# Kernel optimization log

Hardware: AMD Instinct MI355X
Metric: run time of the kernel (lower is better)

Reference implementation:

```python
import jax, jax.numpy as jnp
import numpy as np

NEG = -1e30  # log-zero surrogate (avoid -inf for stable grads)


def ctc_neg_log_like(log_probs, targets, input_lengths, target_lengths):
    """Standard CTC (blank=0) negative log-likelihood, mean over batch.
    Math-equivalent to k2 topo-compile + intersect_dense + log-semiring tot_scores.
    log_probs: [B,T,C] logits or log-probs (re-normalized, as GradExpNormalize does).
    """
    lp = jax.nn.log_softmax(log_probs, axis=-1)
    B, T, C = lp.shape
    S = targets.shape[1]
    L = 2 * S + 1  # blank-interleaved extended label sequence length
    ext = jnp.zeros((B, L), jnp.int32).at[:, 1::2].set(targets.astype(jnp.int32))
    prev2 = jnp.pad(ext[:, :-2], ((0, 0), (2, 0)), constant_values=-1)
    can_skip = (ext != prev2) & (ext != 0)  # skip transition allowed

    lp_tb = jnp.moveaxis(lp, 1, 0)  # [T,B,C] for scan over time
    start = jnp.full((B, L), NEG, lp.dtype).at[:, 0].set(0.0).at[:, 1].set(0.0)
    alpha0 = start + jnp.take_along_axis(lp_tb[0], ext, axis=1)  # [B,L]

    def step(alpha, xs):
        lp_t, t = xs
        emit_t = jnp.take_along_axis(lp_t, ext, axis=1)  # [B,L]
        s1 = jnp.pad(alpha[:, :-1], ((0, 0), (1, 0)), constant_values=NEG)
        s2 = jnp.where(can_skip,
                       jnp.pad(alpha[:, :-2], ((0, 0), (2, 0)), constant_values=NEG),
                       NEG)
        new = jnp.logaddexp(jnp.logaddexp(alpha, s1), s2) + emit_t
        # freeze alpha once past this utterance's length
        new = jnp.where((t < input_lengths)[:, None], new, alpha)
        return new, None

    ts = jnp.arange(1, T, dtype=jnp.int32)
    alpha, _ = jax.lax.scan(step, alpha0, (lp_tb[1:], ts))

    idx1 = (2 * target_lengths).astype(jnp.int32)
    idx2 = jnp.maximum(2 * target_lengths - 1, 0).astype(jnp.int32)
    a1 = jnp.take_along_axis(alpha, idx1[:, None], axis=1)[:, 0]
    a2 = jnp.take_along_axis(alpha, idx2[:, None], axis=1)[:, 0]
    a2 = jnp.where(target_lengths > 0, a2, NEG)
    tot_scores = jnp.logaddexp(a1, a2)  # per-utterance log-likelihood
    return -jnp.mean(tot_scores)  # reduction='mean'


def setup_inputs() -> dict:
    key = jax.random.key(0)
    k1, k2, k3, k4 = jax.random.split(key, 4)
    B, T, C, S = 64, 2048, 1024, 256
    log_probs = jax.random.normal(k1, (B, T, C), dtype=jnp.float32)
    targets = 1 + jax.random.randint(k2, (B, S), 0, C - 1, dtype=jnp.int32)  # labels in [1, C)
    input_lengths = jax.random.randint(k3, (B,), T // 2, T + 1, dtype=jnp.int32)
    target_lengths = jax.random.randint(k4, (B,), S // 2, S + 1, dtype=jnp.int32)
    return {"log_probs": log_probs, "targets": targets,
            "input_lengths": input_lengths, "target_lengths": target_lengths}


def reference(log_probs, targets, input_lengths, target_lengths):
    return ctc_neg_log_like(log_probs, targets, input_lengths, target_lengths)
```

## Files before the change

kernel.cpp:

```cpp
#include <hip/hip_runtime.h>
#include <math.h>

typedef __attribute__((ext_vector_type(4))) float f32x4;

#define SB() __builtin_amdgcn_sched_barrier(0)
#define WAITV(n)                                              \
  do {                                                        \
    asm volatile("s_waitcnt vmcnt(" #n ")" ::: "memory");     \
    SB();                                                     \
  } while (0)
#define LD4(dst, ptr, OFF)                                           \
  asm volatile("global_load_dwordx4 %0, %1, off offset:" OFF         \
               : "=v"(dst) : "v"(ptr) : "memory")
#define LD1(dst, ptr, OFF)                                           \
  asm volatile("global_load_dword %0, %1, off offset:" OFF           \
               : "=v"(dst) : "v"(ptr) : "memory")

__device__ inline float wave_max64(float v) {
#pragma unroll
  for (int off = 32; off > 0; off >>= 1) v = fmaxf(v, __shfl_xor(v, off, 64));
  return v;
}
__device__ inline float wave_sum64(float v) {
#pragma unroll
  for (int off = 32; off > 0; off >>= 1) v += __shfl_xor(v, off, 64);
  return v;
}
__device__ inline float wave_max_dpp(float x) {
  int xi = __float_as_int(x);
  x = fmaxf(x, __int_as_float(__builtin_amdgcn_update_dpp(xi, xi, 0x111, 0xf, 0xf, false)));
  xi = __float_as_int(x);
  x = fmaxf(x, __int_as_float(__builtin_amdgcn_update_dpp(xi, xi, 0x112, 0xf, 0xf, false)));
  xi = __float_as_int(x);
  x = fmaxf(x, __int_as_float(__builtin_amdgcn_update_dpp(xi, xi, 0x114, 0xf, 0xf, false)));
  xi = __float_as_int(x);
  x = fmaxf(x, __int_as_float(__builtin_amdgcn_update_dpp(xi, xi, 0x118, 0xf, 0xf, false)));
  xi = __float_as_int(x);
  x = fmaxf(x, __int_as_float(__builtin_amdgcn_update_dpp(xi, xi, 0x142, 0xa, 0xf, false)));
  xi = __float_as_int(x);
  x = fmaxf(x, __int_as_float(__builtin_amdgcn_update_dpp(xi, xi, 0x143, 0xc, 0xf, false)));
  return __int_as_float(__builtin_amdgcn_readlane(__float_as_int(x), 63));
}
__device__ inline float lane_shr1(float x) {
  return __int_as_float(__builtin_amdgcn_update_dpp(
      0, __float_as_int(x), 0x138, 0xf, 0xf, true));
}

__global__ __launch_bounds__(256) void k1_gather(
    const float* __restrict__ lp, const int* __restrict__ targets,
    float* __restrict__ gw, int t0, int T, int Tc, int RB, int S) {
  __shared__ __align__(16) float rowbuf4[4][1024];
  const int w = threadIdx.x >> 6;
  const int lane = threadIdx.x & 63;
  const int tloc = blockIdx.x * 4 + w;
  const int b = blockIdx.y;
  const int t = t0 + tloc;
  const int4 tg4 = *(const int4*)(targets + (size_t)b * S + 4 * lane);
  float* rowbuf = rowbuf4[w];

  const float* row = lp + ((size_t)b * T + t) * 1024;
  const float4 v0 = *(const float4*)(row + 4 * lane);
  const float4 v1 = *(const float4*)(row + 256 + 4 * lane);
  const float4 v2 = *(const float4*)(row + 512 + 4 * lane);
  const float4 v3 = *(const float4*)(row + 768 + 4 * lane);
  float mx = fmaxf(fmaxf(fmaxf(v0.x, v0.y), fmaxf(v0.z, v0.w)),
                   fmaxf(fmaxf(v1.x, v1.y), fmaxf(v1.z, v1.w)));
  mx = fmaxf(mx, fmaxf(fmaxf(fmaxf(v2.x, v2.y), fmaxf(v2.z, v2.w)),
                       fmaxf(fmaxf(v3.x, v3.y), fmaxf(v3.z, v3.w))));
  mx = wave_max64(mx);
  float sm = __expf(v0.x - mx) + __expf(v0.y - mx) + __expf(v0.z - mx) +
             __expf(v0.w - mx) + __expf(v1.x - mx) + __expf(v1.y - mx) +
             __expf(v1.z - mx) + __expf(v1.w - mx) + __expf(v2.x - mx) +
             __expf(v2.y - mx) + __expf(v2.z - mx) + __expf(v2.w - mx) +
             __expf(v3.x - mx) + __expf(v3.y - mx) + __expf(v3.z - mx) +
             __expf(v3.w - mx);
  sm = wave_sum64(sm);
  const float lse = mx + __logf(sm);
  *(float4*)(rowbuf + 4 * lane) = v0;
  *(float4*)(rowbuf + 256 + 4 * lane) = v1;
  *(float4*)(rowbuf + 512 + 4 * lane) = v2;
  *(float4*)(rowbuf + 768 + 4 * lane) = v3;
  const float e0 = __expf(rowbuf[tg4.x] - lse);
  const float e1 = __expf(rowbuf[tg4.y] - lse);
  const float e2 = __expf(rowbuf[tg4.z] - lse);
  const float e3 = __expf(rowbuf[tg4.w] - lse);
  float* gr = gw + ((size_t)b * RB + tloc) * 264;
  *(float4*)(gr + 4 * lane) = make_float4(e0, e1, e2, e3);
  if (lane == 0) gr[256] = __expf(rowbuf[0] - lse);
}

#define DECL8(P)                                                     \
  f32x4 P##v0, P##v1, P##v2, P##v3, P##v4, P##v5, P##v6, P##v7;      \
  float P##q0, P##q1, P##q2, P##q3, P##q4, P##q5, P##q6, P##q7;

#define ISS8(P)                                                      \
  do {                                                               \
    LD4(P##v0, gpA_, "0");    LD1(P##q0, gqA_, "0");                 \
    LD4(P##v1, gpA_, "1056"); LD1(P##q1, gqA_, "1056");              \
    LD4(P##v2, gpA_, "2112"); LD1(P##q2, gqA_, "2112");              \
    LD4(P##v3, gpA_, "3168"); LD1(P##q3, gqA_, "3168");              \
    LD4(P##v4, gpB_, "0");    LD1(P##q4, gqB_, "0");                 \
    LD4(P##v5, gpB_, "1056"); LD1(P##q5, gqB_, "1056");              \
    LD4(P##v6, gpB_, "2112"); LD1(P##q6, gqB_, "2112");              \
    LD4(P##v7, gpB_, "3168"); LD1(P##q7, gqB_, "3168");              \
    gpA_ += 2112; gqA_ += 2112; gpB_ += 2112; gqB_ += 2112;          \
  } while (0)

#define KSR(pv, qv)                                              \
  {                                                              \
    const float hm1 = lane_shr1(a7);                             \
    const float n0 = (a0 + hm1) * (qv);                          \
    const float n1 = __fmaf_rn(sk1, hm1, a1 + a0) * (pv).x;      \
    const float n2 = (a2 + a1) * (qv);                           \
    const float n3 = __fmaf_rn(sk3, a1, a3 + a2) * (pv).y;       \
    const float n4 = (a4 + a3) * (qv);                           \
    const float n5 = __fmaf_rn(sk5, a3, a5 + a4) * (pv).z;       \
    const float n6 = (a6 + a5) * (qv);                           \
    const float n7 = __fmaf_rn(sk7, a5, a7 + a6) * (pv).w;       \
    const float n8 = (a8 + a7) * (qv);                           \
    a0 = n0; a1 = n1; a2 = n2; a3 = n3; a4 = n4;                 \
    a5 = n5; a6 = n6; a7 = n7; a8 = n8;                          \
  }

#define RESC()                                                            \
  {                                                                       \
    float m_ = fmaxf(fmaxf(fmaxf(fmaxf(a0, a1), fmaxf(a2, a3)),           \
                           fmaxf(fmaxf(a4, a5), fmaxf(a6, a7))), a8);     \
    m_ = wave_max_dpp(m_);                                                \
    const int e_ =                                                        \
        (m_ > 0.f) ? (int)((__float_as_uint(m_) >> 23) & 255u) - 127 : 0; \
    a0 = ldexpf(a0, -e_); a1 = ldexpf(a1, -e_); a2 = ldexpf(a2, -e_);     \
    a3 = ldexpf(a3, -e_); a4 = ldexpf(a4, -e_); a5 = ldexpf(a5, -e_);     \
    a6 = ldexpf(a6, -e_); a7 = ldexpf(a7, -e_); a8 = ldexpf(a8, -e_);     \
    E += e_;                                                              \
  }

#define COMP8(P, rem)                                            \
  do {                                                           \
    if ((rem) >= 8) {                                            \
      KSR(P##v0, P##q0) KSR(P##v1, P##q1) KSR(P##v2, P##q2)      \
      KSR(P##v3, P##q3) KSR(P##v4, P##q4) KSR(P##v5, P##q5)      \
      KSR(P##v6, P##q6) KSR(P##v7, P##q7) RESC()                 \
    } else {                                                     \
      KSR(P##v0, P##q0)                                          \
      if ((rem) > 1) KSR(P##v1, P##q1)                           \
      if ((rem) > 2) KSR(P##v2, P##q2)                           \
      if ((rem) > 3) KSR(P##v3, P##q3)                           \
      if ((rem) > 4) KSR(P##v4, P##q4)                           \
      if ((rem) > 5) KSR(P##v5, P##q5)                           \
      if ((rem) > 6) KSR(P##v6, P##q6)                           \
      RESC()                                                     \
    }                                                            \
  } while (0)

template <int TSREL>
__global__ __launch_bounds__(64, 1) void k2_alpha(
    const float* __restrict__ gw, const int* __restrict__ targets,
    const int* __restrict__ in_len, const int* __restrict__ tgt_len,
    float* __restrict__ alpha_g, int* __restrict__ exp_g,
    float* __restrict__ tot, int t0, int Tc, int RB, int S, int is_last) {
  __shared__ float fin[520];
  const int b = blockIdx.x;
  const int lane = threadIdx.x;
  const float* gb = gw + (size_t)b * RB * 264;
  const int len = in_len[b];
  const int tl = tgt_len[b];
  const int* tg = targets + (size_t)b * S;
  const int4 mytg = *(const int4*)(tg + 4 * lane);
  const int tgm1 = (lane > 0) ? tg[4 * lane - 1] : -1;
  const float sk1 = (lane > 0 && mytg.x != tgm1) ? 1.f : 0.f;
  const float sk3 = (mytg.y != mytg.x) ? 1.f : 0.f;
  const float sk5 = (mytg.z != mytg.y) ? 1.f : 0.f;
  const float sk7 = (mytg.w != mytg.z) ? 1.f : 0.f;

  float a0 = 0.f, a1 = 0.f, a2 = 0.f, a3 = 0.f, a4 = 0.f, a5 = 0.f, a6 = 0.f,
        a7 = 0.f, a8 = 0.f;
  int E = 0;
  if (TSREL) {
    if (lane == 0) { a0 = gb[256]; a1 = gb[0]; }
  } else {
    const float* ap = alpha_g + (size_t)b * 520 + 8 * lane;
    a0 = ap[0]; a1 = ap[1]; a2 = ap[2]; a3 = ap[3];
    a4 = ap[4]; a5 = ap[5]; a6 = ap[6]; a7 = ap[7];
    a8 = (lane == 63) ? alpha_g[(size_t)b * 520 + 512] : 0.f;
    E = exp_g[b];
  }

  const int t_hi = min(t0 + Tc, len);
  int N = t_hi - (t0 + TSREL);
  if (N < 0) N = 0;
  const int G = (N + 7) >> 3;

  const float* gpA_ = gb + (size_t)TSREL * 264 + 4 * lane;
  const float* gqA_ = gb + (size_t)TSREL * 264 + 256;
  const float* gpB_ = gpA_ + 1056;
  const float* gqB_ = gqA_ + 1056;

  DECL8(A) DECL8(B) DECL8(C)

  asm volatile("s_waitcnt vmcnt(0) lgkmcnt(0)" ::: "memory");
  SB();
  ISS8(A); ISS8(B); ISS8(C);

  for (int g = 0; g < G; g += 3) {
    WAITV(32);
    COMP8(A, N - 8 * g);
    ISS8(A);
    if (g + 1 < G) {
      WAITV(32);
      COMP8(B, N - 8 * (g + 1));
      ISS8(B);
    }
    if (g + 2 < G) {
      WAITV(32);
      COMP8(C, N - 8 * (g + 2));
      ISS8(C);
    }
  }
  WAITV(0);

  if (is_last) {
    fin[8 * lane + 0] = a0; fin[8 * lane + 1] = a1;
    fin[8 * lane + 2] = a2; fin[8 * lane + 3] = a3;
    fin[8 * lane + 4] = a4; fin[8 * lane + 5] = a5;
    fin[8 * lane + 6] = a6; fin[8 * lane + 7] = a7;
    if (lane == 63) fin[512] = a8;
    asm volatile("s_waitcnt lgkmcnt(0)" ::: "memory");
    SB();
    if (lane == 0) {
      const int i1 = 2 * tl;
      const int i2 = (2 * tl - 1 > 0) ? (2 * tl - 1) : 0;
      float v = fin[i1] + ((tl > 0) ? fin[i2] : 0.f);
      v = fmaxf(v, 1e-37f);
      tot[b] = logf(v) + (float)E * 0.6931471805599453f;
    }
  } else {
    float* ap = alpha_g + (size_t)b * 520 + 8 * lane;
    ap[0] = a0; ap[1] = a1; ap[2] = a2; ap[3] = a3;
    ap[4] = a4; ap[5] = a5; ap[6] = a6; ap[7] = a7;
    if (lane == 63) alpha_g[(size_t)b * 520 + 512] = a8;
    if (lane == 0) exp_g[b] = E;
  }
}

__global__ void k3_mean(const float* __restrict__ tot, float* __restrict__ out,
                        int B) {
  float v = (threadIdx.x < B) ? tot[threadIdx.x] : 0.0f;
  v = wave_sum64(v);
  if (threadIdx.x == 0) out[0] = -v / (float)B;
}

extern "C" void kernel_launch(void* const* d_in, const int* in_sizes, int n_in,
                              void* d_out, int out_size, void* d_ws,
                              size_t ws_size, hipStream_t stream) {
  const float* lp = (const float*)d_in[0];
  const int* targets = (const int*)d_in[1];
  const int* in_len = (const int*)d_in[2];
  const int* tgt_len = (const int*)d_in[3];
  float* out = (float*)d_out;

  const int B = in_sizes[2];
  const int S = in_sizes[1] / B;
  const int C = 1024;
  const int T = (int)((size_t)in_sizes[0] / ((size_t)B * C));

  const size_t headf = 64 + 64 + (size_t)64 * 520;
  int Tc = T, RB = 0;
  for (;;) {
    RB = Tc + 56;
    const size_t need = headf * 4 + (size_t)64 * RB * 1056;
    if (need <= ws_size || Tc <= 64) break;
    Tc >>= 1;
  }

  float* tot = (float*)d_ws;
  int* exp_g = (int*)(tot + 64);
  float* alpha_g = (float*)(exp_g + 64);
  float* gw = alpha_g + (size_t)64 * 520;

  const int nch = (T + Tc - 1) / Tc;
  for (int c = 0; c < nch; ++c) {
    const int t0 = c * Tc;
    k1_gather<<<dim3(Tc / 4, B), 256, 0, stream>>>(lp, targets, gw, t0, T, Tc,
                                                   RB, S);
    const int last = (c == nch - 1) ? 1 : 0;
    if (c == 0)
      k2_alpha<1><<<B, 64, 0, stream>>>(gw, targets, in_len, tgt_len, alpha_g,
                                        exp_g, tot, t0, Tc, RB, S, last);
    else
      k2_alpha<0><<<B, 64, 0, stream>>>(gw, targets, in_len, tgt_len, alpha_g,
                                        exp_g, tot, t0, Tc, RB, S, last);
  }
  k3_mean<<<1, 64, 0, stream>>>(tot, out, B);
}
```

Measured before the change: 265.9 us.

## Overlap gather of next chunk with alpha recursion via fused double-buffered kernel

Splits time into fixed chunks of up to 512 steps with two gather buffers, and launches a fused kernel per chunk. In it, 64 blocks run the alpha recursion on the previous chunk while the remaining blocks run the log-softmax gather for the next chunk. The goal is to hide the serial, latency-bound recursion behind the bandwidth-bound gather, which previously ran back to back. It also pads rows to 272 floats, cuts the load pipeline from three stages to two, and raises wave priority for the recursion blocks. The cost is more kernel launches and possible contention between the recursion waves and the gather waves on the same device.

```diff
diff --git a/kernel.cpp b/kernel.cpp
--- a/kernel.cpp
+++ b/kernel.cpp
@@ -46,17 +46,16 @@
       0, __float_as_int(x), 0x138, 0xf, 0xf, true));
 }
 
-__global__ __launch_bounds__(256) void k1_gather(
+__device__ __forceinline__ void k1_body(
     const float* __restrict__ lp, const int* __restrict__ targets,
-    float* __restrict__ gw, int t0, int T, int Tc, int RB, int S) {
-  __shared__ __align__(16) float rowbuf4[4][1024];
+    float* __restrict__ gw, int t0, int T, int Tc, int CB, int S,
+    int b, int tq, float* rowbuf) {
+  const int lane = threadIdx.x & 63;
   const int w = threadIdx.x >> 6;
-  const int lane = threadIdx.x & 63;
-  const int tloc = blockIdx.x * 4 + w;
-  const int b = blockIdx.y;
+  const int tloc = tq * 4 + w;
   const int t = t0 + tloc;
+  if (t >= T) return;
   const int4 tg4 = *(const int4*)(targets + (size_t)b * S + 4 * lane);
-  float* rowbuf = rowbuf4[w];
 
   const float* row = lp + ((size_t)b * T + t) * 1024;
   const float4 v0 = *(const float4*)(row + 4 * lane);
@@ -84,9 +83,17 @@
   const float e1 = __expf(rowbuf[tg4.y] - lse);
   const float e2 = __expf(rowbuf[tg4.z] - lse);
   const float e3 = __expf(rowbuf[tg4.w] - lse);
-  float* gr = gw + ((size_t)b * RB + tloc) * 264;
+  float* gr = gw + ((size_t)b * CB + tloc) * 272;
   *(float4*)(gr + 4 * lane) = make_float4(e0, e1, e2, e3);
   if (lane == 0) gr[256] = __expf(rowbuf[0] - lse);
+}
+
+__global__ __launch_bounds__(256) void k1_std(
+    const float* __restrict__ lp, const int* __restrict__ targets,
+    float* __restrict__ gw, int t0, int T, int Tc, int CB, int S) {
+  __shared__ __align__(16) float rowbuf4[4][1024];
+  k1_body(lp, targets, gw, t0, T, Tc, CB, S, blockIdx.y, blockIdx.x,
+          rowbuf4[threadIdx.x >> 6]);
 }
 
 #define DECL8(P)                                                     \
@@ -96,14 +103,14 @@
 #define ISS8(P)                                                      \
   do {                                                               \
     LD4(P##v0, gpA_, "0");    LD1(P##q0, gqA_, "0");                 \
-    LD4(P##v1, gpA_, "1056"); LD1(P##q1, gqA_, "1056");              \
-    LD4(P##v2, gpA_, "2112"); LD1(P##q2, gqA_, "2112");              \
-    LD4(P##v3, gpA_, "3168"); LD1(P##q3, gqA_, "3168");              \
+    LD4(P##v1, gpA_, "1088"); LD1(P##q1, gqA_, "1088");              \
+    LD4(P##v2, gpA_, "2176"); LD1(P##q2, gqA_, "2176");              \
+    LD4(P##v3, gpA_, "3264"); LD1(P##q3, gqA_, "3264");              \
     LD4(P##v4, gpB_, "0");    LD1(P##q4, gqB_, "0");                 \
-    LD4(P##v5, gpB_, "1056"); LD1(P##q5, gqB_, "1056");              \
-    LD4(P##v6, gpB_, "2112"); LD1(P##q6, gqB_, "2112");              \
-    LD4(P##v7, gpB_, "3168"); LD1(P##q7, gqB_, "3168");              \
-    gpA_ += 2112; gqA_ += 2112; gpB_ += 2112; gqB_ += 2112;          \
+    LD4(P##v5, gpB_, "1088"); LD1(P##q5, gqB_, "1088");              \
+    LD4(P##v6, gpB_, "2176"); LD1(P##q6, gqB_, "2176");              \
+    LD4(P##v7, gpB_, "3264"); LD1(P##q7, gqB_, "3264");              \
+    gpA_ += 2176; gqA_ += 2176; gpB_ += 2176; gqB_ += 2176;          \
   } while (0)
 
 #define KSR(pv, qv)                                              \
@@ -153,16 +160,13 @@
     }                                                            \
   } while (0)
 
-template <int TSREL>
-__global__ __launch_bounds__(64, 1) void k2_alpha(
-    const float* __restrict__ gw, const int* __restrict__ targets,
+template <int R0, int LAST>
+__device__ __forceinline__ void k2_body(
+    const float* __restrict__ gb, const int* __restrict__ targets,
     const int* __restrict__ in_len, const int* __restrict__ tgt_len,
     float* __restrict__ alpha_g, int* __restrict__ exp_g,
-    float* __restrict__ tot, int t0, int Tc, int RB, int S, int is_last) {
-  __shared__ float fin[520];
-  const int b = blockIdx.x;
-  const int lane = threadIdx.x;
-  const float* gb = gw + (size_t)b * RB * 264;
+    float* __restrict__ tot, int b, int t0, int Tc, int S) {
+  const int lane = threadIdx.x & 63;
   const int len = in_len[b];
   const int tl = tgt_len[b];
   const int* tg = targets + (size_t)b * S;
@@ -176,7 +180,7 @@
   float a0 = 0.f, a1 = 0.f, a2 = 0.f, a3 = 0.f, a4 = 0.f, a5 = 0.f, a6 = 0.f,
         a7 = 0.f, a8 = 0.f;
   int E = 0;
-  if (TSREL) {
+  if (R0) {
     if (lane == 0) { a0 = gb[256]; a1 = gb[0]; }
   } else {
     const float* ap = alpha_g + (size_t)b * 520 + 8 * lane;
@@ -187,39 +191,37 @@
   }
 
   const int t_hi = min(t0 + Tc, len);
-  int N = t_hi - (t0 + TSREL);
+  int N = t_hi - (t0 + R0);
   if (N < 0) N = 0;
   const int G = (N + 7) >> 3;
 
-  const float* gpA_ = gb + (size_t)TSREL * 264 + 4 * lane;
-  const float* gqA_ = gb + (size_t)TSREL * 264 + 256;
-  const float* gpB_ = gpA_ + 1056;
-  const float* gqB_ = gqA_ + 1056;
-
-  DECL8(A) DECL8(B) DECL8(C)
-
+  const float* gpA_ = gb + (size_t)R0 * 272 + 4 * lane;
+  const float* gqA_ = gb + (size_t)R0 * 272 + 256;
+  const float* gpB_ = gpA_ + 1088;
+  const float* gqB_ = gqA_ + 1088;
+
+  DECL8(A) DECL8(B)
+
+  __builtin_amdgcn_s_setprio(1);
   asm volatile("s_waitcnt vmcnt(0) lgkmcnt(0)" ::: "memory");
   SB();
-  ISS8(A); ISS8(B); ISS8(C);
-
-  for (int g = 0; g < G; g += 3) {
-    WAITV(32);
+  ISS8(A); ISS8(B);
+
+  for (int g = 0; g < G; g += 2) {
+    WAITV(16);
     COMP8(A, N - 8 * g);
     ISS8(A);
     if (g + 1 < G) {
-      WAITV(32);
+      WAITV(16);
       COMP8(B, N - 8 * (g + 1));
       ISS8(B);
     }
-    if (g + 2 < G) {
-      WAITV(32);
-      COMP8(C, N - 8 * (g + 2));
-      ISS8(C);
-    }
   }
   WAITV(0);
-
-  if (is_last) {
+  __builtin_amdgcn_s_setprio(0);
+
+  if constexpr (LAST) {
+    __shared__ float fin[520];
     fin[8 * lane + 0] = a0; fin[8 * lane + 1] = a1;
     fin[8 * lane + 2] = a2; fin[8 * lane + 3] = a3;
     fin[8 * lane + 4] = a4; fin[8 * lane + 5] = a5;
@@ -243,6 +245,38 @@
   }
 }
 
+template <int R0, int LAST>
+__global__ __launch_bounds__(64, 1) void k2_std(
+    const float* __restrict__ gbuf, const int* __restrict__ targets,
+    const int* __restrict__ in_len, const int* __restrict__ tgt_len,
+    float* __restrict__ alpha_g, int* __restrict__ exp_g,
+    float* __restrict__ tot, int t0, int Tc, int CB, int S) {
+  k2_body<R0, LAST>(gbuf + (size_t)blockIdx.x * CB * 272, targets, in_len,
+                    tgt_len, alpha_g, exp_g, tot, blockIdx.x, t0, Tc, S);
+}
+
+template <int R0>
+__global__ __launch_bounds__(256, 1) void fused_k(
+    const float* __restrict__ lp, const int* __restrict__ targets,
+    const int* __restrict__ in_len, const int* __restrict__ tgt_len,
+    float* __restrict__ alpha_g, int* __restrict__ exp_g,
+    float* __restrict__ tot, const float* __restrict__ gprev,
+    float* __restrict__ gcur, int t0k2, int t0k1, int T, int Tc, int CB,
+    int S, int TQ4) {
+  __shared__ __align__(16) float rowbuf4[4][1024];
+  if (blockIdx.x < 64) {
+    if (threadIdx.x >= 64) return;
+    k2_body<R0, 0>(gprev + (size_t)blockIdx.x * CB * 272, targets, in_len,
+                   tgt_len, alpha_g, exp_g, tot, blockIdx.x, t0k2, Tc, S);
+    return;
+  }
+  const int id = blockIdx.x - 64;
+  const int b = id / TQ4;
+  const int tq = id - b * TQ4;
+  k1_body(lp, targets, gcur, t0k1, T, Tc, CB, S, b, tq,
+          rowbuf4[threadIdx.x >> 6]);
+}
+
 __global__ void k3_mean(const float* __restrict__ tot, float* __restrict__ out,
                         int B) {
   float v = (threadIdx.x < B) ? tot[threadIdx.x] : 0.0f;
@@ -265,31 +299,50 @@
   const int T = (int)((size_t)in_sizes[0] / ((size_t)B * C));
 
   const size_t headf = 64 + 64 + (size_t)64 * 520;
-  int Tc = T, RB = 0;
-  for (;;) {
-    RB = Tc + 56;
-    const size_t need = headf * 4 + (size_t)64 * RB * 1056;
-    if (need <= ws_size || Tc <= 64) break;
+  int Tc = 512;
+  if (Tc > T) Tc = T;
+  while (Tc > 64) {
+    const size_t need =
+        headf * 4 + 2 * (size_t)64 * (Tc + 64) * 272 * 4;
+    if (need <= ws_size) break;
     Tc >>= 1;
   }
+  const int CB = Tc + 64;
+  const int nch = (T + Tc - 1) / Tc;
+  const int TQ4 = Tc / 4;
 
   float* tot = (float*)d_ws;
   int* exp_g = (int*)(tot + 64);
   float* alpha_g = (float*)(exp_g + 64);
-  float* gw = alpha_g + (size_t)64 * 520;
-
-  const int nch = (T + Tc - 1) / Tc;
-  for (int c = 0; c < nch; ++c) {
-    const int t0 = c * Tc;
-    k1_gather<<<dim3(Tc / 4, B), 256, 0, stream>>>(lp, targets, gw, t0, T, Tc,
-                                                   RB, S);
-    const int last = (c == nch - 1) ? 1 : 0;
-    if (c == 0)
-      k2_alpha<1><<<B, 64, 0, stream>>>(gw, targets, in_len, tgt_len, alpha_g,
-                                        exp_g, tot, t0, Tc, RB, S, last);
-    else
-      k2_alpha<0><<<B, 64, 0, stream>>>(gw, targets, in_len, tgt_len, alpha_g,
-                                        exp_g, tot, t0, Tc, RB, S, last);
+  float* g0 = alpha_g + (size_t)64 * 520;
+  const size_t BUF = (size_t)64 * CB * 272;
+  float* gbuf[2] = {g0, g0 + BUF};
+
+  if (nch == 1) {
+    k1_std<<<dim3(TQ4, B), 256, 0, stream>>>(lp, targets, gbuf[0], 0, T, Tc,
+                                             CB, S);
+    k2_std<1, 1><<<B, 64, 0, stream>>>(gbuf[0], targets, in_len, tgt_len,
+                                       alpha_g, exp_g, tot, 0, Tc, CB, S);
+  } else {
+    k1_std<<<dim3(TQ4, B), 256, 0, stream>>>(lp, targets, gbuf[0], 0, T, Tc,
+                                             CB, S);
+    for (int c = 1; c < nch; ++c) {
+      const int t0k2 = (c - 1) * Tc;
+      const int t0k1 = c * Tc;
+      const dim3 grid(64 + TQ4 * B);
+      if (c == 1)
+        fused_k<1><<<grid, 256, 0, stream>>>(
+            lp, targets, in_len, tgt_len, alpha_g, exp_g, tot,
+            gbuf[(c - 1) & 1], gbuf[c & 1], t0k2, t0k1, T, Tc, CB, S, TQ4);
+      else
+        fused_k<0><<<grid, 256, 0, stream>>>(
+            lp, targets, in_len, tgt_len, alpha_g, exp_g, tot,
+            gbuf[(c - 1) & 1], gbuf[c & 1], t0k2, t0k1, T, Tc, CB, S, TQ4);
+    }
+    const int cl = nch - 1;
+    k2_std<0, 1><<<B, 64, 0, stream>>>(gbuf[cl & 1], targets, in_len, tgt_len,
+                                       alpha_g, exp_g, tot, cl * Tc, Tc, CB,
+                                       S);
   }
   k3_mean<<<1, 64, 0, stream>>>(tot, out, B);
 }
```

After: 233.5 us (median of 2 runs). -12.2%, faster.
